# Performance work log

Measured on AMD Instinct MI355X. Metric: run time of the kernel, lower is better.

## Reference

```python
import jax, jax.numpy as jnp
import numpy as np

B, N1, N2, C1, C2, MLP_OUT = 16, 4096, 1024, 128, 256, 256


def setup_inputs() -> dict:
    key = jax.random.key(0)
    k = jax.random.split(key, 8)
    xyz1 = jax.random.normal(k[0], (B, N1, 3), dtype=jnp.float32)
    feat1 = jax.random.normal(k[1], (B, N1, C1), dtype=jnp.float32)
    xyz2 = jax.random.normal(k[2], (B, N2, 3), dtype=jnp.float32)
    feat2 = jax.random.normal(k[3], (B, N2, C2), dtype=jnp.float32)
    d_in = C1 + C2
    W1 = jax.random.normal(k[4], (d_in, MLP_OUT), dtype=jnp.float32) / np.sqrt(d_in)
    b1 = jnp.zeros((MLP_OUT,), dtype=jnp.float32)
    W2 = jax.random.normal(k[5], (MLP_OUT, MLP_OUT), dtype=jnp.float32) / np.sqrt(MLP_OUT)
    b2 = jnp.zeros((MLP_OUT,), dtype=jnp.float32)
    return {"xyz1": xyz1, "feat1": feat1, "xyz2": xyz2, "feat2": feat2,
            "W1": W1, "b1": b1, "W2": W2, "b2": b2}


def reference(xyz1, feat1, xyz2, feat2, W1, b1, W2, b2):
    # squared pairwise distances [B, N1, N2]
    dists = jnp.sum((xyz1[:, :, None, :] - xyz2[:, None, :, :]) ** 2, axis=-1)
    # 3 nearest neighbors (smallest distances)
    neg_d3, idx = jax.lax.top_k(-dists, 3)      # [B, N1, 3]
    d3 = jnp.maximum(-neg_d3, 1e-10)
    w = 1.0 / d3
    w = w / jnp.sum(w, axis=-1, keepdims=True)   # [B, N1, 3]
    # gather neighbor features: [B, N1, 3, C2]
    neighbor_feats = jax.vmap(lambda f, i: f[i])(feat2, idx)
    interpolated = jnp.sum(w[..., None] * neighbor_feats, axis=2)  # [B, N1, C2]
    new_feat = jnp.concatenate([interpolated, feat1], axis=-1)     # [B, N1, C2+C1]
    h = jax.nn.relu(new_feat @ W1 + b1)
    return jax.nn.relu(h @ W2 + b2)
```

## Files before the change

### kernel.cpp

```cpp
#include <hip/hip_runtime.h>
#include <cstdint>
#include <cstddef>

typedef unsigned short ushort_t;
typedef unsigned int uint_t;

typedef __bf16 bf16x8 __attribute__((ext_vector_type(8)));
typedef float floatx4 __attribute__((ext_vector_type(4)));

#define B_ 16
#define N1_ 4096
#define N2_ 1024
#define C1_ 128
#define C2_ 256
#define DIN_ 384
#define DOUT_ 256
#define M_ (B_ * N1_)


__device__ __forceinline__ ushort_t f2bf(float f) {
  unsigned int u = __builtin_bit_cast(unsigned int, f);
  u = (u + 0x7fffu + ((u >> 16) & 1u)) >> 16;
  return (ushort_t)u;
}

__device__ __forceinline__ void gload_lds16(const void* g, void* s) {
  __builtin_amdgcn_global_load_lds(
      (__attribute__((address_space(1))) void*)(void*)g,
      (__attribute__((address_space(3))) void*)s, 16, 0, 0);
}

__device__ __forceinline__ void ins3(float& d0, float& d1, float& d2,
                                     int& i0, int& i1, int& i2,
                                     float d, int p) {
  bool c0 = d < d0, c1 = d < d1, c2 = d < d2;
  d2 = c1 ? d1 : (c2 ? d : d2);
  i2 = c1 ? i1 : (c2 ? p : i2);
  d1 = c0 ? d0 : (c1 ? d : d1);
  i1 = c0 ? i0 : (c1 ? p : i1);
  d0 = c0 ? d : d0;
  i0 = c0 ? p : i0;
}


__global__ __launch_bounds__(256) void prep_kernel(
    const float* __restrict__ W1, const float* __restrict__ W2,
    ushort_t* __restrict__ W1t, ushort_t* __restrict__ W2t) {
  int tid = blockIdx.x * 256 + threadIdx.x;
  if (tid < DOUT_ * DIN_) {
    int n = tid / DIN_;
    int k = tid - n * DIN_;
    W1t[tid] = f2bf(W1[(size_t)k * DOUT_ + n]);
  }
  if (tid < DOUT_ * DOUT_) {
    int n = tid >> 8;
    int k = tid & 255;
    W2t[tid] = f2bf(W2[(size_t)k * DOUT_ + n]);
  }
}


__global__ __launch_bounds__(256) void knn_kernel(
    const float* __restrict__ xyz1, const float* __restrict__ xyz2,
    int* __restrict__ idx_out, float* __restrict__ w_out) {
  __shared__ float xs[N2_], ys[N2_], zs[N2_];
  int b = blockIdx.x >> 6;
  int n1base = (blockIdx.x & 63) << 6;
  const float* p2 = xyz2 + (size_t)b * N2_ * 3;
  for (int i = threadIdx.x; i < N2_; i += 256) {
    xs[i] = p2[i * 3 + 0];
    ys[i] = p2[i * 3 + 1];
    zs[i] = p2[i * 3 + 2];
  }
  __syncthreads();

  int g = threadIdx.x >> 2;
  int sub = threadIdx.x & 3;
  int row = b * N1_ + n1base + g;
  const float* p1 = xyz1 + (size_t)row * 3;
  float x1 = p1[0], y1 = p1[1], z1 = p1[2];

  float d0 = 3.0e38f, d1 = 3.0e38f, d2 = 3.0e38f;
  int i0 = 0, i1 = 0, i2 = 0;

  for (int t = 0; t < N2_ / 4; ++t) {
    int p = sub + 4 * t;
    float dx = x1 - xs[p];
    float dy = y1 - ys[p];
    float dz = z1 - zs[p];
    float d = dx * dx + dy * dy + dz * dz;
    ins3(d0, d1, d2, i0, i1, i2, d, p);
  }

#pragma unroll
  for (int m = 1; m <= 2; m <<= 1) {
    float e0 = __shfl_xor(d0, m), e1 = __shfl_xor(d1, m), e2 = __shfl_xor(d2, m);
    int j0 = __shfl_xor(i0, m), j1 = __shfl_xor(i1, m), j2 = __shfl_xor(i2, m);
    ins3(d0, d1, d2, i0, i1, i2, e0, j0);
    ins3(d0, d1, d2, i0, i1, i2, e1, j1);
    ins3(d0, d1, d2, i0, i1, i2, e2, j2);
  }

  if (sub == 0) {
    float r0 = 1.0f / fmaxf(d0, 1e-10f);
    float r1 = 1.0f / fmaxf(d1, 1e-10f);
    float r2 = 1.0f / fmaxf(d2, 1e-10f);
    float s = 1.0f / (r0 + r1 + r2);
    int base = row * 3;
    idx_out[base + 0] = i0;
    idx_out[base + 1] = i1;
    idx_out[base + 2] = i2;
    w_out[base + 0] = r0 * s;
    w_out[base + 1] = r1 * s;
    w_out[base + 2] = r2 * s;
  }
}


__global__ __launch_bounds__(256) void build_kernel(
    const float* __restrict__ feat1, const float* __restrict__ feat2,
    const int* __restrict__ idx, const float* __restrict__ w,
    ushort_t* __restrict__ A1) {
  int wave = threadIdx.x >> 6;
  int lane = threadIdx.x & 63;
  int row = blockIdx.x * 4 + wave;
  int b = row >> 12;

  const int* ip = idx + (size_t)row * 3;
  const float* wp = w + (size_t)row * 3;
  int i0 = ip[0], i1 = ip[1], i2 = ip[2];
  float w0 = wp[0], w1 = wp[1], w2 = wp[2];

  const float4* f0 = (const float4*)(feat2 + ((size_t)b * N2_ + i0) * C2_);
  const float4* f1 = (const float4*)(feat2 + ((size_t)b * N2_ + i1) * C2_);
  const float4* f2 = (const float4*)(feat2 + ((size_t)b * N2_ + i2) * C2_);
  float4 a = f0[lane];
  float4 c = f1[lane];
  float4 d = f2[lane];
  float vx = w0 * a.x + w1 * c.x + w2 * d.x;
  float vy = w0 * a.y + w1 * c.y + w2 * d.y;
  float vz = w0 * a.z + w1 * c.z + w2 * d.z;
  float vw = w0 * a.w + w1 * c.w + w2 * d.w;

  ushort_t* orow = A1 + (size_t)row * DIN_;
  uint_t lo = (uint_t)f2bf(vx) | ((uint_t)f2bf(vy) << 16);
  uint_t hi = (uint_t)f2bf(vz) | ((uint_t)f2bf(vw) << 16);
  ((uint2*)orow)[lane] = make_uint2(lo, hi);

  const float2* g1 = (const float2*)(feat1 + (size_t)row * C1_);
  float2 t = g1[lane];
  uint_t pk = (uint_t)f2bf(t.x) | ((uint_t)f2bf(t.y) << 16);
  *(uint_t*)(orow + C2_ + lane * 2) = pk;
}


template <int K, bool OUT_BF16>
__global__ __launch_bounds__(256) void gemm_kernel(
    const ushort_t* __restrict__ A, const ushort_t* __restrict__ Bt,
    const float* __restrict__ bias, void* __restrict__ out) {
  __shared__ ushort_t As[128 * 32];
  __shared__ ushort_t Bs[128 * 32];
  const int m0 = blockIdx.x * 128;
  const int n0 = blockIdx.y * 128;
  const int wave = threadIdx.x >> 6;
  const int lane = threadIdx.x & 63;
  const int wm = wave & 1;
  const int wn = wave >> 1;

  floatx4 acc[4][4];
#pragma unroll
  for (int i = 0; i < 4; ++i)
#pragma unroll
    for (int j = 0; j < 4; ++j) acc[i][j] = (floatx4)0.0f;

  const int a_off = (wm * 64 + (lane & 15)) * 32 + (lane >> 4) * 8;
  const int b_off = (wn * 64 + (lane & 15)) * 32 + (lane >> 4) * 8;

  for (int kt = 0; kt < K; kt += 32) {
    __syncthreads();
#pragma unroll
    for (int i = 0; i < 2; ++i) {
      int e = (wave * 2 + i) * 512 + lane * 8;
      int r = e >> 5, c = e & 31;
      gload_lds16(A + (size_t)(m0 + r) * K + kt + c, &As[e]);
      gload_lds16(Bt + (size_t)(n0 + r) * K + kt + c, &Bs[e]);
    }
    __syncthreads();

    bf16x8 af[4], bfr[4];
#pragma unroll
    for (int i = 0; i < 4; ++i) af[i] = *(const bf16x8*)&As[a_off + i * 512];
#pragma unroll
    for (int j = 0; j < 4; ++j) bfr[j] = *(const bf16x8*)&Bs[b_off + j * 512];
#pragma unroll
    for (int i = 0; i < 4; ++i)
#pragma unroll
      for (int j = 0; j < 4; ++j)
        acc[i][j] =
            __builtin_amdgcn_mfma_f32_16x16x32_bf16(af[i], bfr[j], acc[i][j], 0, 0, 0);
  }

#pragma unroll
  for (int j = 0; j < 4; ++j) {
    int col = n0 + wn * 64 + j * 16 + (lane & 15);
    float bv = bias[col];
#pragma unroll
    for (int i = 0; i < 4; ++i) {
      int rbase = m0 + wm * 64 + i * 16 + ((lane >> 4) << 2);
#pragma unroll
      for (int r = 0; r < 4; ++r) {
        float v = acc[i][j][r] + bv;
        v = v > 0.0f ? v : 0.0f;
        size_t off = (size_t)(rbase + r) * DOUT_ + col;
        if constexpr (OUT_BF16)
          ((ushort_t*)out)[off] = f2bf(v);
        else
          ((float*)out)[off] = v;
      }
    }
  }
}


constexpr size_t OFF_W1T = 0;
constexpr size_t OFF_W2T = OFF_W1T + 196608;
constexpr size_t OFF_IDX = OFF_W2T + 131072;
constexpr size_t OFF_W = OFF_IDX + 786432;
constexpr size_t OFF_A1 = OFF_W + 786432;
constexpr size_t OFF_H = OFF_A1 + 50331648;
constexpr size_t WS_TOTAL = OFF_H + 33554432;

extern "C" void kernel_launch(void* const* d_in, const int* in_sizes, int n_in,
                              void* d_out, int out_size, void* d_ws, size_t ws_size,
                              hipStream_t stream) {
  const float* xyz1 = (const float*)d_in[0];
  const float* feat1 = (const float*)d_in[1];
  const float* xyz2 = (const float*)d_in[2];
  const float* feat2 = (const float*)d_in[3];
  const float* W1 = (const float*)d_in[4];
  const float* b1 = (const float*)d_in[5];
  const float* W2 = (const float*)d_in[6];
  const float* b2 = (const float*)d_in[7];

  if (ws_size < WS_TOTAL) return;

  char* ws = (char*)d_ws;
  ushort_t* W1t = (ushort_t*)(ws + OFF_W1T);
  ushort_t* W2t = (ushort_t*)(ws + OFF_W2T);
  int* idx = (int*)(ws + OFF_IDX);
  float* w = (float*)(ws + OFF_W);
  ushort_t* A1 = (ushort_t*)(ws + OFF_A1);
  ushort_t* H = (ushort_t*)(ws + OFF_H);

  prep_kernel<<<384, 256, 0, stream>>>(W1, W2, W1t, W2t);
  knn_kernel<<<B_ * (N1_ / 64), 256, 0, stream>>>(xyz1, xyz2, idx, w);
  build_kernel<<<M_ / 4, 256, 0, stream>>>(feat1, feat2, idx, w, A1);
  gemm_kernel<DIN_, true>
      <<<dim3(M_ / 128, DOUT_ / 128), 256, 0, stream>>>(A1, W1t, b1, H);
  gemm_kernel<DOUT_, false>
      <<<dim3(M_ / 128, DOUT_ / 128), 256, 0, stream>>>(H, W2t, b2, (float*)d_out);
}
```

Baseline: 223.0 us.

## Widen GEMM N-tile to full 256 columns and speed up KNN top-3 selection

The KNN kernel now splits each query across 8 lanes instead of 4 and stores xyz2 as float4 in LDS so each point takes one read. It keeps the top-3 with fmed3/fmin and merges lane results with an index-aware tie-break. Each GEMM block now covers all 256 output columns, so every A tile is loaded once instead of twice, at the cost of twice the accumulators per wave and a larger B tile in LDS. This raises register pressure and launch_bounds now requests 2 blocks per unit.

```diff
diff --git a/kernel.cpp b/kernel.cpp
--- a/kernel.cpp
+++ b/kernel.cpp
@@ -30,18 +30,6 @@
       (__attribute__((address_space(3))) void*)s, 16, 0, 0);
 }
 
-__device__ __forceinline__ void ins3(float& d0, float& d1, float& d2,
-                                     int& i0, int& i1, int& i2,
-                                     float d, int p) {
-  bool c0 = d < d0, c1 = d < d1, c2 = d < d2;
-  d2 = c1 ? d1 : (c2 ? d : d2);
-  i2 = c1 ? i1 : (c2 ? p : i2);
-  d1 = c0 ? d0 : (c1 ? d : d1);
-  i1 = c0 ? i0 : (c1 ? p : i1);
-  d0 = c0 ? d : d0;
-  i0 = c0 ? p : i0;
-}
-
 
 __global__ __launch_bounds__(256) void prep_kernel(
     const float* __restrict__ W1, const float* __restrict__ W2,
@@ -60,51 +48,80 @@
 }
 
 
+__device__ __forceinline__ void ins_exact(float& s0, float& s1, float& s2,
+                                          int& i0, int& i1, int& i2,
+                                          float d, int p) {
+  float ns2 = __builtin_amdgcn_fmed3f(d, s1, s2);
+  float ns1 = __builtin_amdgcn_fmed3f(d, s0, s1);
+  float ns0 = fminf(d, s0);
+  bool c0 = d < s0, c1 = d < s1, c2 = d < s2;
+  i2 = c1 ? i1 : (c2 ? p : i2);
+  i1 = c0 ? i0 : (c1 ? p : i1);
+  i0 = c0 ? p : i0;
+  s0 = ns0; s1 = ns1; s2 = ns2;
+}
+
+__device__ __forceinline__ void ins_merge(float& s0, float& s1, float& s2,
+                                          int& i0, int& i1, int& i2,
+                                          float e, int j) {
+  bool t0 = (e < s0) || (e == s0 && j < i0);
+  bool t1 = (e < s1) || (e == s1 && j < i1);
+  bool t2 = (e < s2) || (e == s2 && j < i2);
+  s2 = t1 ? s1 : (t2 ? e : s2);
+  i2 = t1 ? i1 : (t2 ? j : i2);
+  s1 = t0 ? s0 : (t1 ? e : s1);
+  i1 = t0 ? i0 : (t1 ? j : i1);
+  s0 = t0 ? e : s0;
+  i0 = t0 ? j : i0;
+}
+
 __global__ __launch_bounds__(256) void knn_kernel(
     const float* __restrict__ xyz1, const float* __restrict__ xyz2,
     int* __restrict__ idx_out, float* __restrict__ w_out) {
-  __shared__ float xs[N2_], ys[N2_], zs[N2_];
-  int b = blockIdx.x >> 6;
-  int n1base = (blockIdx.x & 63) << 6;
+  __shared__ float4 xs4[N2_];
+  int b = blockIdx.x >> 7;
+  int n1base = (blockIdx.x & 127) << 5;
   const float* p2 = xyz2 + (size_t)b * N2_ * 3;
   for (int i = threadIdx.x; i < N2_; i += 256) {
-    xs[i] = p2[i * 3 + 0];
-    ys[i] = p2[i * 3 + 1];
-    zs[i] = p2[i * 3 + 2];
+    const float* s = p2 + 3 * i;
+    xs4[i] = make_float4(s[0], s[1], s[2], 0.0f);
   }
   __syncthreads();
 
-  int g = threadIdx.x >> 2;
-  int sub = threadIdx.x & 3;
+  int g = threadIdx.x >> 3;
+  int sub = threadIdx.x & 7;
   int row = b * N1_ + n1base + g;
   const float* p1 = xyz1 + (size_t)row * 3;
   float x1 = p1[0], y1 = p1[1], z1 = p1[2];
 
-  float d0 = 3.0e38f, d1 = 3.0e38f, d2 = 3.0e38f;
+  float s0 = 3.0e38f, s1 = 3.0e38f, s2 = 3.0e38f;
   int i0 = 0, i1 = 0, i2 = 0;
 
-  for (int t = 0; t < N2_ / 4; ++t) {
-    int p = sub + 4 * t;
-    float dx = x1 - xs[p];
-    float dy = y1 - ys[p];
-    float dz = z1 - zs[p];
+  int p = sub;
+#pragma unroll 8
+  for (int t = 0; t < N2_ / 8; ++t) {
+    float4 q = xs4[p];
+    float dx = x1 - q.x;
+    float dy = y1 - q.y;
+    float dz = z1 - q.z;
     float d = dx * dx + dy * dy + dz * dz;
-    ins3(d0, d1, d2, i0, i1, i2, d, p);
-  }
-
-#pragma unroll
-  for (int m = 1; m <= 2; m <<= 1) {
-    float e0 = __shfl_xor(d0, m), e1 = __shfl_xor(d1, m), e2 = __shfl_xor(d2, m);
+    ins_exact(s0, s1, s2, i0, i1, i2, d, p);
+    p += 8;
+  }
+
+#pragma unroll
+  for (int m = 1; m <= 4; m <<= 1) {
+    float e0 = __shfl_xor(s0, m), e1 = __shfl_xor(s1, m), e2 = __shfl_xor(s2, m);
     int j0 = __shfl_xor(i0, m), j1 = __shfl_xor(i1, m), j2 = __shfl_xor(i2, m);
-    ins3(d0, d1, d2, i0, i1, i2, e0, j0);
-    ins3(d0, d1, d2, i0, i1, i2, e1, j1);
-    ins3(d0, d1, d2, i0, i1, i2, e2, j2);
+    ins_merge(s0, s1, s2, i0, i1, i2, e0, j0);
+    ins_merge(s0, s1, s2, i0, i1, i2, e1, j1);
+    ins_merge(s0, s1, s2, i0, i1, i2, e2, j2);
   }
 
   if (sub == 0) {
-    float r0 = 1.0f / fmaxf(d0, 1e-10f);
-    float r1 = 1.0f / fmaxf(d1, 1e-10f);
-    float r2 = 1.0f / fmaxf(d2, 1e-10f);
+    float r0 = 1.0f / fmaxf(s0, 1e-10f);
+    float r1 = 1.0f / fmaxf(s1, 1e-10f);
+    float r2 = 1.0f / fmaxf(s2, 1e-10f);
     float s = 1.0f / (r0 + r1 + r2);
     int base = row * 3;
     idx_out[base + 0] = i0;
@@ -155,54 +172,59 @@
 
 
 template <int K, bool OUT_BF16>
-__global__ __launch_bounds__(256) void gemm_kernel(
+__global__ __launch_bounds__(256, 2) void gemm_kernel(
     const ushort_t* __restrict__ A, const ushort_t* __restrict__ Bt,
     const float* __restrict__ bias, void* __restrict__ out) {
   __shared__ ushort_t As[128 * 32];
-  __shared__ ushort_t Bs[128 * 32];
+  __shared__ ushort_t Bs[256 * 32];
   const int m0 = blockIdx.x * 128;
-  const int n0 = blockIdx.y * 128;
-  const int wave = threadIdx.x >> 6;
-  const int lane = threadIdx.x & 63;
+  const int tid = threadIdx.x;
+  const int wave = tid >> 6;
+  const int lane = tid & 63;
   const int wm = wave & 1;
   const int wn = wave >> 1;
 
-  floatx4 acc[4][4];
+  floatx4 acc[4][8];
 #pragma unroll
   for (int i = 0; i < 4; ++i)
 #pragma unroll
-    for (int j = 0; j < 4; ++j) acc[i][j] = (floatx4)0.0f;
+    for (int j = 0; j < 8; ++j) acc[i][j] = (floatx4)0.0f;
 
   const int a_off = (wm * 64 + (lane & 15)) * 32 + (lane >> 4) * 8;
-  const int b_off = (wn * 64 + (lane & 15)) * 32 + (lane >> 4) * 8;
+  const int b_off = (wn * 128 + (lane & 15)) * 32 + (lane >> 4) * 8;
 
   for (int kt = 0; kt < K; kt += 32) {
     __syncthreads();
 #pragma unroll
     for (int i = 0; i < 2; ++i) {
-      int e = (wave * 2 + i) * 512 + lane * 8;
+      int e = (i * 256 + tid) * 8;
       int r = e >> 5, c = e & 31;
       gload_lds16(A + (size_t)(m0 + r) * K + kt + c, &As[e]);
-      gload_lds16(Bt + (size_t)(n0 + r) * K + kt + c, &Bs[e]);
+    }
+#pragma unroll
+    for (int i = 0; i < 4; ++i) {
+      int e = (i * 256 + tid) * 8;
+      int r = e >> 5, c = e & 31;
+      gload_lds16(Bt + (size_t)r * K + kt + c, &Bs[e]);
     }
     __syncthreads();
 
-    bf16x8 af[4], bfr[4];
+    bf16x8 af[4], bfr[8];
 #pragma unroll
     for (int i = 0; i < 4; ++i) af[i] = *(const bf16x8*)&As[a_off + i * 512];
 #pragma unroll
-    for (int j = 0; j < 4; ++j) bfr[j] = *(const bf16x8*)&Bs[b_off + j * 512];
+    for (int j = 0; j < 8; ++j) bfr[j] = *(const bf16x8*)&Bs[b_off + j * 512];
 #pragma unroll
     for (int i = 0; i < 4; ++i)
 #pragma unroll
-      for (int j = 0; j < 4; ++j)
+      for (int j = 0; j < 8; ++j)
         acc[i][j] =
             __builtin_amdgcn_mfma_f32_16x16x32_bf16(af[i], bfr[j], acc[i][j], 0, 0, 0);
   }
 
 #pragma unroll
-  for (int j = 0; j < 4; ++j) {
-    int col = n0 + wn * 64 + j * 16 + (lane & 15);
+  for (int j = 0; j < 8; ++j) {
+    int col = wn * 128 + j * 16 + (lane & 15);
     float bv = bias[col];
 #pragma unroll
     for (int i = 0; i < 4; ++i) {
@@ -253,10 +275,8 @@
   ushort_t* H = (ushort_t*)(ws + OFF_H);
 
   prep_kernel<<<384, 256, 0, stream>>>(W1, W2, W1t, W2t);
-  knn_kernel<<<B_ * (N1_ / 64), 256, 0, stream>>>(xyz1, xyz2, idx, w);
+  knn_kernel<<<B_ * (N1_ / 32), 256, 0, stream>>>(xyz1, xyz2, idx, w);
   build_kernel<<<M_ / 4, 256, 0, stream>>>(feat1, feat2, idx, w, A1);
-  gemm_kernel<DIN_, true>
-      <<<dim3(M_ / 128, DOUT_ / 128), 256, 0, stream>>>(A1, W1t, b1, H);
-  gemm_kernel<DOUT_, false>
-      <<<dim3(M_ / 128, DOUT_ / 128), 256, 0, stream>>>(H, W2t, b2, (float*)d_out);
-}
+  gemm_kernel<DIN_, true><<<M_ / 128, 256, 0, stream>>>(A1, W1t, b1, H);
+  gemm_kernel<DOUT_, false><<<M_ / 128, 256, 0, stream>>>(H, W2t, b2, (float*)d_out);
+}
```

New measurement: 217.4 us. 2.5% less time.
